# Optimization experiments

Hardware: AMD Instinct MI355X
Metric: run time of the kernel (lower is better)

## Reference

```python
import jax, jax.numpy as jnp
import numpy as np

D, NH, NL, NP, DFF = 256, 8, 4, 4, 1024
DH = D // NH
# 4-level FPN of a 1024x1024 image at strides 8/16/32/64 (H, W per level)
SHAPES = np.array([[128, 128], [64, 64], [32, 32], [16, 16]], dtype=np.int32)


def setup_inputs() -> dict:
    ks = jax.random.split(jax.random.key(0), 16)
    B, Lq = 4, 900
    sizes = SHAPES[:, 0] * SHAPES[:, 1]
    Lin = int(sizes.sum())
    starts = np.concatenate([[0], np.cumsum(sizes)[:-1]]).astype(np.int32)
    s = 0.02  # small init so softmax/LN stay well-conditioned

    def w(k, shape):
        return jax.random.normal(k, shape, jnp.float32) * s

    return {
        "tgt": jax.random.normal(ks[0], (Lq, B, D), jnp.float32),
        "tgt_reference_points": jax.random.uniform(ks[1], (Lq, B, NL, 2), jnp.float32),
        "memory": jax.random.normal(ks[2], (Lin, B, D), jnp.float32),
        "W_off": w(ks[3], (NH * NL * NP * 2, D)), "b_off": w(ks[4], (NH * NL * NP * 2,)),
        "W_attn": w(ks[5], (NH * NL * NP, D)), "b_attn": w(ks[6], (NH * NL * NP,)),
        "W_val": w(ks[7], (D, D)), "b_val": w(ks[8], (D,)),
        "W_out": w(ks[9], (D, D)), "b_out": w(ks[10], (D,)),
        "ln1_g": jnp.ones((D,), jnp.float32), "ln1_b": jnp.zeros((D,), jnp.float32),
        "W1": w(ks[11], (DFF, D)), "b1": w(ks[12], (DFF,)),
        "W2": w(ks[13], (D, DFF)), "b2": w(ks[14], (D,)),
        "ln3_g": jnp.ones((D,), jnp.float32), "ln3_b": jnp.zeros((D,), jnp.float32),
        "memory_spatial_shapes": jnp.asarray(SHAPES),
        "memory_level_start_index": jnp.asarray(starts),
        "memory_key_padding_mask": jnp.zeros((B, Lin), jnp.bool_),
    }


def _ln(x, g, b, eps=1e-5):
    mu = x.mean(-1, keepdims=True)
    var = ((x - mu) ** 2).mean(-1, keepdims=True)
    return (x - mu) * jax.lax.rsqrt(var + eps) * g + b


def _bilinear(vl, loc, H, W):
    # vl: (B, NH, H*W, DH); loc: (B, Lq, NH, NP, 2) normalized to [0,1]
    # matches torch grid_sample(mode='bilinear', padding_mode='zeros', align_corners=False)
    B, Lq, nh, P, _ = loc.shape
    x = loc[..., 0] * W - 0.5
    y = loc[..., 1] * H - 0.5
    x0f = jnp.floor(x)
    y0f = jnp.floor(y)
    x0 = x0f.astype(jnp.int32)
    y0 = y0f.astype(jnp.int32)
    wx1 = x - x0f
    wy1 = y - y0f

    def tap(xi, yi, w):
        valid = (xi >= 0) & (xi < W) & (yi >= 0) & (yi < H)
        idx = jnp.clip(yi, 0, H - 1) * W + jnp.clip(xi, 0, W - 1)
        idx = idx.transpose(0, 2, 1, 3).reshape(B, nh, Lq * P)
        ww = (w * valid).transpose(0, 2, 1, 3).reshape(B, nh, Lq * P)
        vals = jnp.take_along_axis(vl, idx[..., None], axis=2)  # (B,NH,Lq*P,DH)
        return vals * ww[..., None]

    acc = (tap(x0, y0, (1 - wx1) * (1 - wy1)) + tap(x0 + 1, y0, wx1 * (1 - wy1))
           + tap(x0, y0 + 1, (1 - wx1) * wy1) + tap(x0 + 1, y0 + 1, wx1 * wy1))
    return acc.reshape(B, nh, Lq, P, DH)


def _msda(q, ref, value, shapes_np, W_off, b_off, W_attn, b_attn, W_out, b_out):
    # q: (B,Lq,D), ref: (B,Lq,NL,2), value: (B,Lin,NH,DH)
    B, Lq, _ = q.shape
    off = (q @ W_off.T + b_off).reshape(B, Lq, NH, NL, NP, 2)
    a = jax.nn.softmax((q @ W_attn.T + b_attn).reshape(B, Lq, NH, NL * NP), axis=-1)
    a = a.reshape(B, Lq, NH, NL, NP)
    norm = jnp.asarray(shapes_np[:, ::-1].copy(), jnp.float32)  # (NL, 2) as (W, H)
    loc = ref[:, :, None, :, None, :] + off / norm[None, None, None, :, None, :]
    sizes = [int(h) * int(w) for h, w in shapes_np]
    starts = np.concatenate([[0], np.cumsum(sizes)[:-1]])
    v = value.transpose(0, 2, 1, 3)  # (B, NH, Lin, DH)
    out = jnp.zeros((B, NH, Lq, DH), q.dtype)
    for l, (H, W) in enumerate(shapes_np):
        vl = v[:, :, int(starts[l]):int(starts[l]) + sizes[l], :]
        sampled = _bilinear(vl, loc[:, :, :, l], int(H), int(W))  # (B,NH,Lq,NP,DH)
        wl = a[:, :, :, l].transpose(0, 2, 1, 3)  # (B,NH,Lq,NP)
        out = out + (sampled * wl[..., None]).sum(3)
    out = out.transpose(0, 2, 1, 3).reshape(B, Lq, D)
    return out @ W_out.T + b_out


def reference(tgt, tgt_reference_points, memory, W_off, b_off, W_attn, b_attn,
              W_val, b_val, W_out, b_out, ln1_g, ln1_b, W1, b1, W2, b2, ln3_g, ln3_b,
              memory_spatial_shapes, memory_level_start_index, memory_key_padding_mask):
    shapes_np = np.asarray(memory_spatial_shapes)  # static level metadata
    q = tgt.transpose(1, 0, 2)                      # (B, Lq, D)
    ref = tgt_reference_points.transpose(1, 0, 2, 3)
    mem = memory.transpose(1, 0, 2)                 # (B, Lin, D)
    B, Lin, _ = mem.shape
    value = mem @ W_val.T + b_val
    value = jnp.where(memory_key_padding_mask[..., None], 0.0, value)
    value = value.reshape(B, Lin, NH, DH)
    ca = _msda(q, ref, value, shapes_np, W_off, b_off, W_attn, b_attn, W_out, b_out)
    # residual + LN (dropout is identity in eval)
    t = _ln(tgt + ca.transpose(1, 0, 2), ln1_g, ln1_b)
    # FFN
    t2 = jax.nn.relu(t @ W1.T + b1) @ W2.T + b2
    return _ln(t + t2, ln3_g, ln3_b)
```

## Files before the change

kernel.cpp:

```cpp
#include <hip/hip_runtime.h>
#include <hip/hip_bf16.h>

#define B_   4
#define LQ_  900
#define D_   256
#define NH_  8
#define DH_  32
#define NL_  4
#define NP_  4
#define DFF_ 1024
#define LIN_ 21760
#define MQ_  (LQ_*B_)
#define MV_  (LIN_*B_)
#define VALBLKS (MV_/32)

typedef __attribute__((ext_vector_type(8))) short bh8;
typedef __attribute__((ext_vector_type(4))) float f32x4;

__device__ __forceinline__ short bf16b(float f) {
    __hip_bfloat16 h = __float2bfloat16(f);
    return *reinterpret_cast<short*>(&h);
}

__device__ __forceinline__ void gload_lds16(const void* g, void* l) {
    __builtin_amdgcn_global_load_lds(
        (const __attribute__((address_space(1))) unsigned int*)g,
        (__attribute__((address_space(3))) unsigned int*)l, 16, 0, 0);
}

__device__ __forceinline__ bh8 af_from_f32(const float* p) {
    float4 v0 = *reinterpret_cast<const float4*>(p);
    float4 v1 = *reinterpret_cast<const float4*>(p + 4);
    return (bh8){ bf16b(v0.x), bf16b(v0.y), bf16b(v0.z), bf16b(v0.w),
                  bf16b(v1.x), bf16b(v1.y), bf16b(v1.z), bf16b(v1.w) };
}

__global__ __launch_bounds__(256)
void wprep_k(const float* __restrict__ Woff, const float* __restrict__ Wattn,
             const float* __restrict__ Wout, const float* __restrict__ W1,
             const float* __restrict__ W2, const float* __restrict__ Wval,
             unsigned char* __restrict__ qkvimg, unsigned char* __restrict__ outimg,
             unsigned char* __restrict__ w1img, unsigned char* __restrict__ w2img,
             unsigned char* __restrict__ valimg)
{
    const int cid = blockIdx.x*256 + threadIdx.x;
    const float* W; unsigned char* img; int KQ, c;
    if      (cid < 8192)  { W=Woff;  img=qkvimg;           KQ=8;  c=cid;       }
    else if (cid < 12288) { W=Wattn; img=qkvimg + 131072;  KQ=8;  c=cid-8192;  }
    else if (cid < 20480) { W=Wout;  img=outimg;           KQ=8;  c=cid-12288; }
    else if (cid < 53248) { W=W1;    img=w1img;            KQ=8;  c=cid-20480; }
    else if (cid < 86016) { W=W2;    img=w2img;            KQ=32; c=cid-53248; }
    else                  { W=Wval;  img=valimg;           KQ=8;  c=cid-86016; }
    const int K   = KQ*32;
    const int n16 = c & 15, g = (c>>4)&3, t = c>>6;
    const int kq  = t & (KQ-1);
    const int ntile = t >> ((KQ==8) ? 3 : 5);
    const int n = ntile*16 + n16, k0 = kq*32 + g*8;
    float4 v0 = *reinterpret_cast<const float4*>(&W[(size_t)n*K + k0]);
    float4 v1 = *reinterpret_cast<const float4*>(&W[(size_t)n*K + k0 + 4]);
    union { short s[8]; uint4 u; } pk;
    pk.s[0]=bf16b(v0.x); pk.s[1]=bf16b(v0.y); pk.s[2]=bf16b(v0.z); pk.s[3]=bf16b(v0.w);
    pk.s[4]=bf16b(v1.x); pk.s[5]=bf16b(v1.y); pk.s[6]=bf16b(v1.z); pk.s[7]=bf16b(v1.w);
    *reinterpret_cast<uint4*>(img + (size_t)(ntile*KQ + kq)*1024 + (g*16+n16)*16) = pk.u;
}

__global__ __launch_bounds__(256, 4)
void valqkv_k(const float* __restrict__ A, const unsigned char* __restrict__ Wimg,
              const float* __restrict__ bias, unsigned short* __restrict__ C,
              const unsigned char* __restrict__ mask,
              const float* __restrict__ tgt, const unsigned char* __restrict__ Qimg,
              const float* __restrict__ b_off, const float* __restrict__ b_attn,
              float* __restrict__ Yoff, float* __restrict__ Yattn)
{
    __shared__ __align__(16) unsigned char Al[32768];

    const int tid  = threadIdx.x;
    const int lane = tid & 63;

    if (blockIdx.x < VALBLKS) {
        const int wc   = tid >> 6;
        const int m0   = blockIdx.x * 32;
        const int r16  = lane & 15;
        const int g    = lane >> 4;

        const unsigned char* Abyte = (const unsigned char*)A;
        const unsigned char* wlane = Wimg + lane*16;

        const int a_row = (tid >> 3) & 31;
        const int a_x   = (tid & 7) * 16;
        const size_t a_src_row = (size_t)(m0 + a_row) * 1024 + (a_x ^ ((a_row & 7) << 4));
        const int a_dst = tid * 16;

#define ISSUE_A(KQ) gload_lds16(Abyte + a_src_row + (KQ)*128, (char*)Al + (KQ)*4096 + a_dst)
#define ISSUE_W(KQ, SLOT)                                                              \
    do { _Pragma("unroll")                                                             \
        for (int i_ = 0; i_ < 4; ++i_)                                                 \
            bfr[SLOT][i_] = *reinterpret_cast<const bh8*>(                             \
                wlane + (size_t)((wc*4 + i_)*8 + (KQ))*1024);                          \
    } while (0)

        bh8 bfr[3][4];

        ISSUE_A(0);
        ISSUE_W(0, 0);
        ISSUE_W(1, 1);
        ISSUE_A(1);
        ISSUE_A(2);

        f32x4 acc[2][4];
        #pragma unroll
        for (int i = 0; i < 2; ++i)
            #pragma unroll
            for (int j = 0; j < 4; ++j) acc[i][j] = (f32x4){0.f,0.f,0.f,0.f};

        #pragma unroll
        for (int kq = 0; kq < 8; ++kq) {
            if (kq < 6)      asm volatile("s_waitcnt vmcnt(6)" ::: "memory");
            else if (kq == 6) asm volatile("s_waitcnt vmcnt(5)" ::: "memory");
            else              asm volatile("s_waitcnt vmcnt(0)" ::: "memory");
            __builtin_amdgcn_s_barrier();

            bh8 af[2];
            #pragma unroll
            for (int mf = 0; mf < 2; ++mf) {
                const int row = mf*16 + r16;
                const int swz = (row & 7) << 4;
                const char* base = (const char*)Al + kq*4096 + row*128;
                float4 v0 = *reinterpret_cast<const float4*>(base + ((g*32     ) ^ swz));
                float4 v1 = *reinterpret_cast<const float4*>(base + ((g*32 + 16) ^ swz));
                af[mf] = (bh8){ bf16b(v0.x), bf16b(v0.y), bf16b(v0.z), bf16b(v0.w),
                                bf16b(v1.x), bf16b(v1.y), bf16b(v1.z), bf16b(v1.w) };
            }

            if (kq == 0) { ISSUE_W(2, 2); ISSUE_A(3); }
            if (kq == 1) { ISSUE_W(3, 0); ISSUE_A(4); }
            if (kq == 2) { ISSUE_W(4, 1); ISSUE_A(5); }
            if (kq == 3) { ISSUE_W(5, 2); ISSUE_A(6); }
            if (kq == 4) { ISSUE_W(6, 0); ISSUE_A(7); }
            if (kq == 5) { ISSUE_W(7, 1); }

            #pragma unroll
            for (int mf = 0; mf < 2; ++mf)
                #pragma unroll
                for (int i = 0; i < 4; ++i)
                    acc[mf][i] = __builtin_amdgcn_mfma_f32_16x16x32_bf16(af[mf], bfr[kq % 3][i], acc[mf][i], 0, 0, 0);
        }
#undef ISSUE_A
#undef ISSUE_W

        float bv[4];
        #pragma unroll
        for (int i = 0; i < 4; ++i) bv[i] = bias[wc*64 + i*16 + r16];

        #pragma unroll
        for (int mf = 0; mf < 2; ++mf) {
            #pragma unroll
            for (int r = 0; r < 4; ++r) {
                const int gm = m0 + mf*16 + g*4 + r;
                const bool z = mask[(gm & 3)*LIN_ + (gm >> 2)] != 0;
                #pragma unroll
                for (int i = 0; i < 4; ++i) {
                    float v = acc[mf][i][r] + bv[i];
                    if (z) v = 0.f;
                    C[(size_t)gm*256 + wc*64 + i*16 + r16] = (unsigned short)bf16b(v);
                }
            }
        }
    } else {
        const int w   = tid >> 6;
        const int m16 = lane & 15, g = lane >> 4;
        const int m0  = (blockIdx.x - VALBLKS) * 16;

        bh8 af[8];
        #pragma unroll
        for (int kq = 0; kq < 8; ++kq)
            af[kq] = af_from_f32(&tgt[(size_t)(m0 + m16)*256 + kq*32 + g*8]);

        f32x4 acc[6];
        #pragma unroll
        for (int i = 0; i < 6; ++i) acc[i] = (f32x4){0.f,0.f,0.f,0.f};

        #pragma unroll
        for (int i = 0; i < 6; ++i) {
            const int nt = w*6 + i;
            #pragma unroll
            for (int kq = 0; kq < 8; ++kq) {
                bh8 bf = *reinterpret_cast<const bh8*>(Qimg + (size_t)(nt*8 + kq)*1024 + lane*16);
                acc[i] = __builtin_amdgcn_mfma_f32_16x16x32_bf16(af[kq], bf, acc[i], 0, 0, 0);
            }
        }

        #pragma unroll
        for (int i = 0; i < 6; ++i) {
            const int nt = w*6 + i;
            const int j  = nt*16 + m16;
            #pragma unroll
            for (int r = 0; r < 4; ++r) {
                const int m = m0 + g*4 + r;
                if (nt < 16) Yoff[(size_t)m*256 + j] = acc[i][r] + b_off[j];
                else         Yattn[(size_t)m*128 + (j-256)] = acc[i][r] + b_attn[j-256];
            }
        }
    }
}

__global__ __launch_bounds__(1024, 2)
void outffn_k(const float* __restrict__ Amsda, const unsigned char* __restrict__ Oimg,
              const float* __restrict__ b_out, const float* __restrict__ res,
              const float* __restrict__ l1g, const float* __restrict__ l1b,
              const unsigned char* __restrict__ W1img, const float* __restrict__ b1,
              const unsigned char* __restrict__ W2img, const float* __restrict__ b2,
              const float* __restrict__ l3g, const float* __restrict__ l3b,
              float* __restrict__ Yout)
{
    __shared__ float sln[16][256];
    __shared__ __align__(16) short hl[2][16*272];

    const int tid = threadIdx.x, lane = tid & 63, w = tid >> 6;
    const int m16 = lane & 15, g = lane >> 4;
    const int m0 = blockIdx.x * 16;

    {
        bh8 af[8];
        #pragma unroll
        for (int kq = 0; kq < 8; ++kq)
            af[kq] = af_from_f32(&Amsda[(size_t)(m0 + m16)*256 + kq*32 + g*8]);

        f32x4 acc = (f32x4){0.f,0.f,0.f,0.f};
        #pragma unroll
        for (int kq = 0; kq < 8; ++kq) {
            bh8 bf = *reinterpret_cast<const bh8*>(Oimg + (size_t)(w*8 + kq)*1024 + lane*16);
            acc = __builtin_amdgcn_mfma_f32_16x16x32_bf16(af[kq], bf, acc, 0, 0, 0);
        }

        const int j = w*16 + m16;
        #pragma unroll
        for (int r = 0; r < 4; ++r) {
            const int ml = g*4 + r;
            sln[ml][j] = acc[r] + b_out[j] + res[(size_t)(m0 + ml)*256 + j];
        }
    }
    __syncthreads();

    {
        const int row = w, l2 = lane;
        float v[4], s1 = 0.f, s2 = 0.f;
        #pragma unroll
        for (int c = 0; c < 4; ++c) {
            v[c] = sln[row][l2 + c*64];
            s1 += v[c]; s2 += v[c]*v[c];
        }
        #pragma unroll
        for (int o = 32; o >= 1; o >>= 1) {
            s1 += __shfl_xor(s1, o, 64);
            s2 += __shfl_xor(s2, o, 64);
        }
        const float mu  = s1 * (1.f/256.f);
        const float var = s2 * (1.f/256.f) - mu*mu;
        const float is  = rsqrtf(var + 1e-5f);
        #pragma unroll
        for (int c = 0; c < 4; ++c) {
            const int jj = l2 + c*64;
            sln[row][jj] = (v[c] - mu) * is * l1g[jj] + l1b[jj];
        }
    }
    __syncthreads();

    bh8 af1[8];
    #pragma unroll
    for (int kq = 0; kq < 8; ++kq)
        af1[kq] = af_from_f32(&sln[m16][kq*32 + g*8]);

    f32x4 yacc = (f32x4){0.f,0.f,0.f,0.f};

    int buf = 0;
    #pragma unroll
    for (int fc = 0; fc < 4; ++fc) {
        const int ftile_g = fc*16 + w;
        f32x4 hacc = (f32x4){0.f,0.f,0.f,0.f};
        #pragma unroll
        for (int kq = 0; kq < 8; ++kq) {
            bh8 bf = *reinterpret_cast<const bh8*>(W1img + (size_t)(ftile_g*8 + kq)*1024 + lane*16);
            hacc = __builtin_amdgcn_mfma_f32_16x16x32_bf16(af1[kq], bf, hacc, 0, 0, 0);
        }
        const float bb = b1[ftile_g*16 + m16];
        #pragma unroll
        for (int r = 0; r < 4; ++r) {
            const float v = fmaxf(hacc[r] + bb, 0.f);
            hl[buf][(g*4 + r)*272 + w*16 + m16] = bf16b(v);
        }
        __syncthreads();
        bh8 a2[8];
        #pragma unroll
        for (int kqf = 0; kqf < 8; ++kqf)
            a2[kqf] = *reinterpret_cast<const bh8*>((const char*)&hl[buf][0]
                + m16*544 + (kqf*32 + g*8)*2);
        #pragma unroll
        for (int kqf = 0; kqf < 8; ++kqf) {
            const int kq2 = fc*8 + kqf;
            bh8 bf = *reinterpret_cast<const bh8*>(W2img + (size_t)(w*32 + kq2)*1024 + lane*16);
            yacc = __builtin_amdgcn_mfma_f32_16x16x32_bf16(a2[kqf], bf, yacc, 0, 0, 0);
        }
        buf ^= 1;
    }

    {
        const int j = w*16 + m16;
        #pragma unroll
        for (int r = 0; r < 4; ++r) {
            const int ml = g*4 + r;
            sln[ml][j] = yacc[r] + b2[j] + sln[ml][j];
        }
    }
    __syncthreads();

    {
        const int row = w, l2 = lane;
        float v[4], s1 = 0.f, s2 = 0.f;
        #pragma unroll
        for (int c = 0; c < 4; ++c) {
            v[c] = sln[row][l2 + c*64];
            s1 += v[c]; s2 += v[c]*v[c];
        }
        #pragma unroll
        for (int o = 32; o >= 1; o >>= 1) {
            s1 += __shfl_xor(s1, o, 64);
            s2 += __shfl_xor(s2, o, 64);
        }
        const float mu  = s1 * (1.f/256.f);
        const float var = s2 * (1.f/256.f) - mu*mu;
        const float is  = rsqrtf(var + 1e-5f);
        #pragma unroll
        for (int c = 0; c < 4; ++c) {
            const int jj = l2 + c*64;
            Yout[(size_t)(m0 + row)*256 + jj] = (v[c] - mu) * is * l3g[jj] + l3b[jj];
        }
    }
}

__global__ __launch_bounds__(256)
void msda_k(const float* __restrict__ off,
            const float* __restrict__ attnlog,
            const float* __restrict__ refp,
            const __hip_bfloat16* __restrict__ value,
            float* __restrict__ out)
{
    const int m = blockIdx.x;
    const int b = m & 3;
    const int d = threadIdx.x;
    const int h = d >> 5;

    __shared__ float s_off[256];
    __shared__ float s_al[128];
    __shared__ float s_ref[NL_*2];
    s_off[d] = off[(size_t)m*256 + d];
    if (d < 128) s_al[d] = attnlog[(size_t)m*128 + d];
    if (d < NL_*2) s_ref[d] = refp[(size_t)m*(NL_*2) + d];
    __syncthreads();

    float mx = -1e30f;
    #pragma unroll
    for (int t = 0; t < 16; ++t) mx = fmaxf(mx, s_al[h*16 + t]);
    float e[16], ssum = 0.f;
    #pragma unroll
    for (int t = 0; t < 16; ++t) { e[t] = __expf(s_al[h*16 + t] - mx); ssum += e[t]; }
    const float inv = 1.f / ssum;

    const int HS[4] = {128, 64, 32, 16};
    const int ST[4] = {0, 16384, 20480, 21504};

    float acc = 0.f;
    #pragma unroll
    for (int l = 0; l < NL_; ++l) {
        const int H = HS[l], W = HS[l], st = ST[l];
        const float rx = s_ref[l*2+0], ry = s_ref[l*2+1];
        #pragma unroll
        for (int p = 0; p < NP_; ++p) {
            const int base = ((h*NL_ + l)*NP_ + p);
            const float a  = e[l*4 + p] * inv;
            const float ox = s_off[base*2+0], oy = s_off[base*2+1];
            const float x = rx*(float)W + ox - 0.5f;
            const float y = ry*(float)H + oy - 0.5f;
            const float x0f = floorf(x), y0f = floorf(y);
            const int x0 = (int)x0f, y0 = (int)y0f;
            const float wx1 = x - x0f, wy1 = y - y0f;
            const float wx0 = 1.f - wx1, wy0 = 1.f - wy1;
            #pragma unroll
            for (int t = 0; t < 4; ++t) {
                const int xi = x0 + (t & 1);
                const int yi = y0 + (t >> 1);
                const float wgt = (t==0 ? wx0*wy0 : t==1 ? wx1*wy0 : t==2 ? wx0*wy1 : wx1*wy1);
                if (xi >= 0 && xi < W && yi >= 0 && yi < H) {
                    const size_t idx = (size_t)(st + yi*W + xi);
                    const float v = __bfloat162float(value[(idx*B_ + b)*D_ + d]);
                    acc = fmaf(a*wgt, v, acc);
                }
            }
        }
    }
    out[(size_t)m*256 + d] = acc;
}

extern "C" void kernel_launch(void* const* d_in, const int* in_sizes, int n_in,
                              void* d_out, int out_size, void* d_ws, size_t ws_size,
                              hipStream_t stream)
{
    const float* tgt    = (const float*)d_in[0];
    const float* refp   = (const float*)d_in[1];
    const float* mem    = (const float*)d_in[2];
    const float* W_off  = (const float*)d_in[3];
    const float* b_off  = (const float*)d_in[4];
    const float* W_attn = (const float*)d_in[5];
    const float* b_attn = (const float*)d_in[6];
    const float* W_val  = (const float*)d_in[7];
    const float* b_val  = (const float*)d_in[8];
    const float* W_out  = (const float*)d_in[9];
    const float* b_out  = (const float*)d_in[10];
    const float* ln1g   = (const float*)d_in[11];
    const float* ln1b   = (const float*)d_in[12];
    const float* W1     = (const float*)d_in[13];
    const float* b1     = (const float*)d_in[14];
    const float* W2     = (const float*)d_in[15];
    const float* b2     = (const float*)d_in[16];
    const float* ln3g   = (const float*)d_in[17];
    const float* ln3b   = (const float*)d_in[18];
    const unsigned char* mask = (const unsigned char*)d_in[21];
    float* out = (float*)d_out;

    char* p = (char*)d_ws;
    __hip_bfloat16* value = (__hip_bfloat16*)p; p += (size_t)MV_*D_*2;
    float* offb = (float*)p; p += (size_t)MQ_*256*4;
    float* attl = (float*)p; p += (size_t)MQ_*128*4;
    float* msda = (float*)p; p += (size_t)MQ_*256*4;
    unsigned char* qkvimg = (unsigned char*)p; p += 196608;
    unsigned char* outimg = (unsigned char*)p; p += 131072;
    unsigned char* w1img  = (unsigned char*)p; p += 524288;
    unsigned char* w2img  = (unsigned char*)p; p += 524288;
    unsigned char* valimg = (unsigned char*)p; p += 131072;
    (void)ws_size; (void)in_sizes; (void)n_in; (void)out_size;

    wprep_k<<<dim3(368), dim3(256), 0, stream>>>(W_off, W_attn, W_out, W1, W2, W_val,
                                                 qkvimg, outimg, w1img, w2img, valimg);
    valqkv_k<<<dim3(VALBLKS + MQ_/16), dim3(256), 0, stream>>>(
        mem, valimg, b_val, (unsigned short*)value, mask,
        tgt, qkvimg, b_off, b_attn, offb, attl);
    msda_k<<<dim3(MQ_), dim3(256), 0, stream>>>(offb, attl, refp, value, msda);
    outffn_k<<<dim3(MQ_/16), dim3(1024), 0, stream>>>(
        msda, outimg, b_out, tgt, ln1g, ln1b,
        w1img, b1, w2img, b2, ln3g, ln3b, out);
}
```

Measured before the change: 115.7 us.

## Split value-projection GEMM across N halves and vectorize MSDA bf16 gathers

The value projection now launches two blocks per 32-row tile, each computing half of the 256 output columns. Each block preloads all of its weight fragments into registers up front instead of streaming them through a rotating three-slot buffer. This doubles the block count and shortens per-block work, at the cost of reading the memory-input tile twice. Separately, the deformable-attention kernel processes two queries per block, with each thread handling two channels via 32-bit bf16 pair loads and a float2 store, halving the gather instruction count.

```diff
diff --git a/kernel.cpp b/kernel.cpp
--- a/kernel.cpp
+++ b/kernel.cpp
@@ -12,7 +12,7 @@
 #define LIN_ 21760
 #define MQ_  (LQ_*B_)
 #define MV_  (LIN_*B_)
-#define VALBLKS (MV_/32)
+#define VALBLKS ((MV_/32)*2)
 
 typedef __attribute__((ext_vector_type(8))) short bh8;
 typedef __attribute__((ext_vector_type(4))) float f32x4;
@@ -78,10 +78,12 @@
     const int lane = tid & 63;
 
     if (blockIdx.x < VALBLKS) {
-        const int wc   = tid >> 6;
-        const int m0   = blockIdx.x * 32;
-        const int r16  = lane & 15;
-        const int g    = lane >> 4;
+        const int wc    = tid >> 6;
+        const int mt    = blockIdx.x >> 1;
+        const int nhalf = blockIdx.x & 1;
+        const int m0    = mt * 32;
+        const int r16   = lane & 15;
+        const int g     = lane >> 4;
 
         const unsigned char* Abyte = (const unsigned char*)A;
         const unsigned char* wlane = Wimg + lane*16;
@@ -92,31 +94,36 @@
         const int a_dst = tid * 16;
 
 #define ISSUE_A(KQ) gload_lds16(Abyte + a_src_row + (KQ)*128, (char*)Al + (KQ)*4096 + a_dst)
-#define ISSUE_W(KQ, SLOT)                                                              \
-    do { _Pragma("unroll")                                                             \
-        for (int i_ = 0; i_ < 4; ++i_)                                                 \
-            bfr[SLOT][i_] = *reinterpret_cast<const bh8*>(                             \
-                wlane + (size_t)((wc*4 + i_)*8 + (KQ))*1024);                          \
-    } while (0)
-
-        bh8 bfr[3][4];
+
+        bh8 wreg[2][8];
+        #pragma unroll
+        for (int i = 0; i < 2; ++i)
+            #pragma unroll
+            for (int kq = 0; kq < 8; ++kq)
+                wreg[i][kq] = *reinterpret_cast<const bh8*>(
+                    wlane + (size_t)((nhalf*8 + wc*2 + i)*8 + kq)*1024);
 
         ISSUE_A(0);
-        ISSUE_W(0, 0);
-        ISSUE_W(1, 1);
         ISSUE_A(1);
         ISSUE_A(2);
 
-        f32x4 acc[2][4];
+        asm volatile("s_waitcnt vmcnt(3)" ::: "memory");
         #pragma unroll
         for (int i = 0; i < 2; ++i)
             #pragma unroll
-            for (int j = 0; j < 4; ++j) acc[i][j] = (f32x4){0.f,0.f,0.f,0.f};
+            for (int kq = 0; kq < 8; ++kq)
+                asm volatile("" : "+v"(wreg[i][kq]));
+
+        f32x4 acc[2][2];
+        #pragma unroll
+        for (int i = 0; i < 2; ++i)
+            #pragma unroll
+            for (int j = 0; j < 2; ++j) acc[i][j] = (f32x4){0.f,0.f,0.f,0.f};
 
         #pragma unroll
         for (int kq = 0; kq < 8; ++kq) {
-            if (kq < 6)      asm volatile("s_waitcnt vmcnt(6)" ::: "memory");
-            else if (kq == 6) asm volatile("s_waitcnt vmcnt(5)" ::: "memory");
+            if (kq < 6)      asm volatile("s_waitcnt vmcnt(2)" ::: "memory");
+            else if (kq == 6) asm volatile("s_waitcnt vmcnt(1)" ::: "memory");
             else              asm volatile("s_waitcnt vmcnt(0)" ::: "memory");
             __builtin_amdgcn_s_barrier();
 
@@ -132,25 +139,19 @@
                                 bf16b(v1.x), bf16b(v1.y), bf16b(v1.z), bf16b(v1.w) };
             }
 
-            if (kq == 0) { ISSUE_W(2, 2); ISSUE_A(3); }
-            if (kq == 1) { ISSUE_W(3, 0); ISSUE_A(4); }
-            if (kq == 2) { ISSUE_W(4, 1); ISSUE_A(5); }
-            if (kq == 3) { ISSUE_W(5, 2); ISSUE_A(6); }
-            if (kq == 4) { ISSUE_W(6, 0); ISSUE_A(7); }
-            if (kq == 5) { ISSUE_W(7, 1); }
+            if (kq < 5) ISSUE_A(kq + 3);
 
             #pragma unroll
             for (int mf = 0; mf < 2; ++mf)
                 #pragma unroll
-                for (int i = 0; i < 4; ++i)
-                    acc[mf][i] = __builtin_amdgcn_mfma_f32_16x16x32_bf16(af[mf], bfr[kq % 3][i], acc[mf][i], 0, 0, 0);
+                for (int i = 0; i < 2; ++i)
+                    acc[mf][i] = __builtin_amdgcn_mfma_f32_16x16x32_bf16(af[mf], wreg[i][kq], acc[mf][i], 0, 0, 0);
         }
 #undef ISSUE_A
-#undef ISSUE_W
-
-        float bv[4];
-        #pragma unroll
-        for (int i = 0; i < 4; ++i) bv[i] = bias[wc*64 + i*16 + r16];
+
+        float bv[2];
+        #pragma unroll
+        for (int i = 0; i < 2; ++i) bv[i] = bias[nhalf*128 + wc*32 + i*16 + r16];
 
         #pragma unroll
         for (int mf = 0; mf < 2; ++mf) {
@@ -159,10 +160,10 @@
                 const int gm = m0 + mf*16 + g*4 + r;
                 const bool z = mask[(gm & 3)*LIN_ + (gm >> 2)] != 0;
                 #pragma unroll
-                for (int i = 0; i < 4; ++i) {
+                for (int i = 0; i < 2; ++i) {
                     float v = acc[mf][i][r] + bv[i];
                     if (z) v = 0.f;
-                    C[(size_t)gm*256 + wc*64 + i*16 + r16] = (unsigned short)bf16b(v);
+                    C[(size_t)gm*256 + nhalf*128 + wc*32 + i*16 + r16] = (unsigned short)bf16b(v);
                 }
             }
         }
@@ -345,40 +346,46 @@
             const __hip_bfloat16* __restrict__ value,
             float* __restrict__ out)
 {
-    const int m = blockIdx.x;
-    const int b = m & 3;
-    const int d = threadIdx.x;
-    const int h = d >> 5;
-
-    __shared__ float s_off[256];
-    __shared__ float s_al[128];
-    __shared__ float s_ref[NL_*2];
-    s_off[d] = off[(size_t)m*256 + d];
-    if (d < 128) s_al[d] = attnlog[(size_t)m*128 + d];
-    if (d < NL_*2) s_ref[d] = refp[(size_t)m*(NL_*2) + d];
+    const int hp = threadIdx.x >> 7;
+    const int dd = threadIdx.x & 127;
+    const int d0 = dd * 2;
+    const int m  = blockIdx.x*2 + hp;
+    const int b  = m & 3;
+    const int h  = dd >> 4;
+
+    __shared__ float s_off[2][256];
+    __shared__ float s_al[2][128];
+    __shared__ float s_ref[2][NL_*2];
+    {
+        const int t2 = threadIdx.x & 127;
+        s_off[hp][t2]       = off[(size_t)m*256 + t2];
+        s_off[hp][t2 + 128] = off[(size_t)m*256 + t2 + 128];
+        if (t2 < 128) s_al[hp][t2] = attnlog[(size_t)m*128 + t2];
+        if (t2 < NL_*2) s_ref[hp][t2] = refp[(size_t)m*(NL_*2) + t2];
+    }
     __syncthreads();
 
     float mx = -1e30f;
     #pragma unroll
-    for (int t = 0; t < 16; ++t) mx = fmaxf(mx, s_al[h*16 + t]);
+    for (int t = 0; t < 16; ++t) mx = fmaxf(mx, s_al[hp][h*16 + t]);
     float e[16], ssum = 0.f;
     #pragma unroll
-    for (int t = 0; t < 16; ++t) { e[t] = __expf(s_al[h*16 + t] - mx); ssum += e[t]; }
+    for (int t = 0; t < 16; ++t) { e[t] = __expf(s_al[hp][h*16 + t] - mx); ssum += e[t]; }
     const float inv = 1.f / ssum;
 
     const int HS[4] = {128, 64, 32, 16};
     const int ST[4] = {0, 16384, 20480, 21504};
 
-    float acc = 0.f;
+    float acc0 = 0.f, acc1 = 0.f;
     #pragma unroll
     for (int l = 0; l < NL_; ++l) {
         const int H = HS[l], W = HS[l], st = ST[l];
-        const float rx = s_ref[l*2+0], ry = s_ref[l*2+1];
+        const float rx = s_ref[hp][l*2+0], ry = s_ref[hp][l*2+1];
         #pragma unroll
         for (int p = 0; p < NP_; ++p) {
             const int base = ((h*NL_ + l)*NP_ + p);
             const float a  = e[l*4 + p] * inv;
-            const float ox = s_off[base*2+0], oy = s_off[base*2+1];
+            const float ox = s_off[hp][base*2+0], oy = s_off[hp][base*2+1];
             const float x = rx*(float)W + ox - 0.5f;
             const float y = ry*(float)H + oy - 0.5f;
             const float x0f = floorf(x), y0f = floorf(y);
@@ -392,13 +399,19 @@
                 const float wgt = (t==0 ? wx0*wy0 : t==1 ? wx1*wy0 : t==2 ? wx0*wy1 : wx1*wy1);
                 if (xi >= 0 && xi < W && yi >= 0 && yi < H) {
                     const size_t idx = (size_t)(st + yi*W + xi);
-                    const float v = __bfloat162float(value[(idx*B_ + b)*D_ + d]);
-                    acc = fmaf(a*wgt, v, acc);
+                    const unsigned int v = *reinterpret_cast<const unsigned int*>(
+                        &value[(idx*B_ + b)*D_ + d0]);
+                    const float f0 = __uint_as_float(v << 16);
+                    const float f1 = __uint_as_float(v & 0xffff0000u);
+                    const float aw = a * wgt;
+                    acc0 = fmaf(aw, f0, acc0);
+                    acc1 = fmaf(aw, f1, acc1);
                 }
             }
         }
     }
-    out[(size_t)m*256 + d] = acc;
+    float2 o2 = { acc0, acc1 };
+    *reinterpret_cast<float2*>(&out[(size_t)m*256 + d0]) = o2;
 }
 
 extern "C" void kernel_launch(void* const* d_in, const int* in_sizes, int n_in,
@@ -444,7 +457,7 @@
     valqkv_k<<<dim3(VALBLKS + MQ_/16), dim3(256), 0, stream>>>(
         mem, valimg, b_val, (unsigned short*)value, mask,
         tgt, qkvimg, b_off, b_attn, offb, attl);
-    msda_k<<<dim3(MQ_), dim3(256), 0, stream>>>(offb, attl, refp, value, msda);
+    msda_k<<<dim3(MQ_/2), dim3(256), 0, stream>>>(offb, attl, refp, value, msda);
     outffn_k<<<dim3(MQ_/16), dim3(1024), 0, stream>>>(
         msda, outimg, b_out, tgt, ln1g, ln1b,
         w1img, b1, w2img, b2, ln3g, ln3b, out);
```

Measured after the change: 112.1 us. 1.03x faster.
